# Kernel tuning notes

Measured on AMD Instinct MI355X. Metric: run time of the kernel, lower is better.

## Reference

```python
import jax, jax.numpy as jnp
import numpy as np
from jax.scipy.special import gammaln

F = 128      # n_atom_basis = n_filters
K = 25       # n_basis_functions
L = 3        # n_interactions
CUTOFF = 5.0
MAX_Z = 100
B, A, NBH = 16, 256, 64


def ssp(x):
    # shifted softplus: log(0.5*e^x + 0.5)
    return jax.nn.softplus(x) - jnp.log(2.0).astype(x.dtype)


def cosine_cutoff(r):
    return jnp.where(r < CUTOFF, 0.5 * (jnp.cos(jnp.pi * r / CUTOFF) + 1.0), 0.0)


def bernstein_basis(r):
    # ExponentialBernsteinPolynomials: Bernstein polys of exp(-r), K functions
    x = jnp.exp(-r)[..., None]                      # [..., 1]
    k = jnp.arange(K, dtype=r.dtype)
    n = jnp.asarray(K - 1, dtype=r.dtype)
    logbinom = gammaln(n + 1) - gammaln(k + 1) - gammaln(n - k + 1)
    eps = 1e-10
    return jnp.exp(logbinom + k * jnp.log(x + eps) + (n - k) * jnp.log(1.0 - x + eps))


def gather_nbh(y, neighbors):
    # y: [B, A, D], neighbors: [B, A, N] -> [B, A, N, D]
    b, a, n = neighbors.shape
    idx = neighbors.reshape(b, a * n)
    out = jnp.take_along_axis(y, idx[:, :, None], axis=1)
    return out.reshape(b, a, n, y.shape[-1])


def setup_inputs() -> dict:
    key = jax.random.key(0)
    ks = jax.random.split(key, 16)
    s = 0.05
    inp = {
        "positions": jax.random.normal(ks[0], (B, A, 3), dtype=jnp.float32) * 3.0,
        "neighbor_mask": jnp.ones((B, A, NBH), dtype=jnp.float32),
        "atom_mask": jnp.ones((B, A), dtype=jnp.float32),
        "emb": jax.random.normal(ks[1], (MAX_Z, F), dtype=jnp.float32) * s,
        "Wfs": jax.random.normal(ks[2], (L, K, F), dtype=jnp.float32) * s,
        "Wfp": jax.random.normal(ks[3], (L, K, F), dtype=jnp.float32) * s,
        "Win": jax.random.normal(ks[4], (L, F, F), dtype=jnp.float32) * s,
        "Wf2o": jax.random.normal(ks[5], (L, F, F), dtype=jnp.float32) * s,
        "bf2o": jnp.zeros((L, F), dtype=jnp.float32),
        "Wd": jax.random.normal(ks[6], (L, F, F), dtype=jnp.float32) * s,
        "bd": jnp.zeros((L, F), dtype=jnp.float32),
        "Wq": jax.random.normal(ks[7], (L, F, F), dtype=jnp.float32) * s,
        "Wk": jax.random.normal(ks[8], (L, F, F), dtype=jnp.float32) * s,
        "Wv": jax.random.normal(ks[9], (L, F, F), dtype=jnp.float32) * s,
        "atomic_numbers": jax.random.randint(ks[10], (B, A), 0, MAX_Z, dtype=jnp.int32),
        "neighbors": jax.random.randint(ks[11], (B, A, NBH), 0, A, dtype=jnp.int32),
    }
    return inp


def reference(positions, neighbor_mask, atom_mask, emb, Wfs, Wfp, Win, Wf2o, bf2o,
              Wd, bd, Wq, Wk, Wv, atomic_numbers, neighbors):
    # embedding (padding_idx=0 means Z=0 rows are just the table row; fine for ref)
    x = emb[atomic_numbers]                              # [B,A,F]

    # AtomDistances (no PBC): gather neighbor positions, distances + directions
    pos_j = gather_nbh(positions, neighbors)             # [B,A,N,3]
    rvec = pos_j - positions[:, :, None, :]
    r = jnp.sqrt(jnp.sum(rvec * rvec, axis=-1) + 1e-12) * neighbor_mask  # [B,A,N]
    dhat = rvec / (r[..., None] + 1e-9)                  # unit directions (l=1 harmonics)

    f = bernstein_basis(r)                               # [B,A,N,K]
    fc = cosine_cutoff(r) * neighbor_mask                # [B,A,N]

    for l in range(L):
        # --- LocalInteraction: angular CFConv (s + p blocks) ---
        Ws = (f @ Wfs[l]) * fc[..., None]                # [B,A,N,F]
        Wp = (f @ Wfp[l]) * fc[..., None]                # [B,A,N,F]
        y = x @ Win[l]                                   # in2f, no bias
        yj = gather_nbh(y, neighbors)                    # [B,A,N,F]
        cs = jnp.sum(yj * Ws, axis=2)                    # s-block scatter-sum [B,A,F]
        tp = jnp.einsum('banm,banf->bamf', dhat, yj * Wp)  # [B,A,3,F]
        cp = jnp.sum(tp * tp, axis=2)                    # rot-invariant p-block [B,A,F]
        v = ssp((cs + cp) @ Wf2o[l] + bf2o[l])           # f2out with shifted softplus
        v = v @ Wd[l] + bd[l]                            # interaction dense

        # --- NonLocalInteraction: masked attention ---
        xm = x * atom_mask[..., None]
        q = ssp(xm @ Wq[l])
        k = ssp(xm @ Wk[l])
        vv = ssp(xm @ Wv[l])
        logits = jnp.einsum('baf,bcf->bac', q, k) / jnp.sqrt(jnp.float32(F))
        logits = logits + (1.0 - atom_mask)[:, None, :] * (-1e9)
        att = jax.nn.softmax(logits, axis=-1)
        n = jnp.einsum('bac,bcf->baf', att, vv) * atom_mask[..., None]

        x = x + v + n                                    # residual update
    return x
```

## Files before the change

kernel.cpp:

```cpp
#include <hip/hip_runtime.h>
#include <hip/hip_bf16.h>
#include <math.h>

#define NB   16
#define NA   256
#define NNBH 64
#define NF   128
#define NK   25
#define NATOM (NB*NA)

typedef __attribute__((ext_vector_type(4))) float f32x4;
typedef __attribute__((ext_vector_type(8))) short bf16x8;

__device__ __constant__ float BINOM_C[25] = {
  1.f, 24.f, 276.f, 2024.f, 10626.f, 42504.f, 134596.f, 346104.f,
  735471.f, 1307504.f, 1961256.f, 2496144.f, 2704156.f, 2496144.f,
  1961256.f, 1307504.f, 735471.f, 346104.f, 134596.f, 42504.f,
  10626.f, 2024.f, 276.f, 24.f, 1.f
};

__device__ __forceinline__ float sspf(float x) {
  float t = (x > 20.f) ? x : log1pf(expf(x));
  return t - 0.69314718055994531f;
}
__device__ __forceinline__ unsigned short f2bf(float x) {
  __hip_bfloat16 h = __float2bfloat16(x);
  return *(unsigned short*)&h;
}

__global__ __launch_bounds__(256) void k_init(
    const float* __restrict__ Win, const float* __restrict__ Wf2o,
    const float* __restrict__ Wd, const float* __restrict__ Wq,
    const float* __restrict__ Wk, const float* __restrict__ Wv,
    const float* __restrict__ Wfs, const float* __restrict__ Wfp,
    __hip_bfloat16* __restrict__ WT, __hip_bfloat16* __restrict__ Wfb) {
  int bid = blockIdx.x, tid = threadIdx.x;
  if (bid < 1152) {
    int idx = bid * 256 + tid;
    int e = idx & 16383; int m = idx >> 14;
    int l = m / 6, wsel = m - l * 6;
    const float* src = (wsel == 0) ? Win : (wsel == 1) ? Wf2o : (wsel == 2) ? Wd
                      : (wsel == 3) ? Wq : (wsel == 4) ? Wk : Wv;
    int k = e >> 7, col = e & 127;
    WT[m * 16384 + col * 128 + k] = __float2bfloat16(src[l * NF * NF + k * NF + col]);
  } else {
    int idx = (bid - 1152) * 256 + tid;
    int k = idx & 31, f = (idx >> 5) & 127, s = (idx >> 12) & 1, l = idx >> 13;
    float v = 0.f;
    if (k < NK) v = (s ? Wfp : Wfs)[l * NK * NF + k * NF + f];
    Wfb[idx] = __float2bfloat16(v);
  }
}

template<int HV>
__global__ __launch_bounds__(256) void k_proj(
    const float* __restrict__ xg, const int* __restrict__ Z,
    const float* __restrict__ emb,
    const float* __restrict__ Cb, const float* __restrict__ Nb,
    const __hip_bfloat16* __restrict__ WTf2o_p, const float* __restrict__ bf2o_p,
    const __hip_bfloat16* __restrict__ WTd_p, const float* __restrict__ bd_p,
    const float* __restrict__ amask, const __hip_bfloat16* __restrict__ WTl,
    float* __restrict__ xout,
    __hip_bfloat16* __restrict__ ybf, __hip_bfloat16* __restrict__ Qw,
    __hip_bfloat16* __restrict__ Kw, __hip_bfloat16* __restrict__ VwT) {
  __shared__ __hip_bfloat16 hLDS[16 * 132];
  __shared__ float xLDS[16 * 133];
  int tid = threadIdx.x;
  int z = tid >> 6, l = tid & 63, lr = l & 15, lg = l >> 4;
  int rbase = blockIdx.x * 16;

  if (HV) {
    bf16x8 cfr[4];
    const float* cr = Cb + (rbase + lr) * NF;
    #pragma unroll
    for (int ks = 0; ks < 4; ks++) {
      int k0 = ks * 32 + lg * 8;
      float4 a = *(const float4*)&cr[k0];
      float4 c = *(const float4*)&cr[k0 + 4];
      bf16x8 t;
      t[0] = (short)f2bf(a.x); t[1] = (short)f2bf(a.y);
      t[2] = (short)f2bf(a.z); t[3] = (short)f2bf(a.w);
      t[4] = (short)f2bf(c.x); t[5] = (short)f2bf(c.y);
      t[6] = (short)f2bf(c.z); t[7] = (short)f2bf(c.w);
      cfr[ks] = t;
    }
    f32x4 hacc[2];
    hacc[0] = (f32x4){0.f, 0.f, 0.f, 0.f};
    hacc[1] = (f32x4){0.f, 0.f, 0.f, 0.f};
    #pragma unroll
    for (int ks = 0; ks < 4; ks++)
      #pragma unroll
      for (int j = 0; j < 2; j++) {
        bf16x8 bfr = *(const bf16x8*)(WTf2o_p + ((2 * z + j) * 16 + lr) * NF + ks * 32 + lg * 8);
        hacc[j] = __builtin_amdgcn_mfma_f32_16x16x32_bf16(cfr[ks], bfr, hacc[j], 0, 0, 0);
      }
    #pragma unroll
    for (int j = 0; j < 2; j++) {
      int col = (2 * z + j) * 16 + lr;
      float bv = bf2o_p[col];
      #pragma unroll
      for (int r = 0; r < 4; r++)
        hLDS[(4 * lg + r) * 132 + col] = __float2bfloat16(sspf(hacc[j][r] + bv));
    }
    __syncthreads();
    bf16x8 hfr[4];
    #pragma unroll
    for (int ks = 0; ks < 4; ks++)
      hfr[ks] = *(const bf16x8*)&hLDS[lr * 132 + ks * 32 + lg * 8];
    f32x4 vacc[2];
    vacc[0] = (f32x4){0.f, 0.f, 0.f, 0.f};
    vacc[1] = (f32x4){0.f, 0.f, 0.f, 0.f};
    #pragma unroll
    for (int ks = 0; ks < 4; ks++)
      #pragma unroll
      for (int j = 0; j < 2; j++) {
        bf16x8 bfr = *(const bf16x8*)(WTd_p + ((2 * z + j) * 16 + lr) * NF + ks * 32 + lg * 8);
        vacc[j] = __builtin_amdgcn_mfma_f32_16x16x32_bf16(hfr[ks], bfr, vacc[j], 0, 0, 0);
      }
    #pragma unroll
    for (int j = 0; j < 2; j++) {
      int col = (2 * z + j) * 16 + lr;
      float bv = bd_p[col];
      #pragma unroll
      for (int r = 0; r < 4; r++) {
        int row = rbase + 4 * lg + r;
        float xv = xg[row * NF + col] + vacc[j][r] + bv + Nb[row * NF + col];
        xout[row * NF + col] = xv;
        xLDS[(4 * lg + r) * 133 + col] = xv;
      }
    }
    __syncthreads();
  } else {
    int rr = tid >> 4, c0 = (tid & 15) * 8;
    int row = rbase + rr;
    const float* er = emb + Z[row] * NF;
    float4 a = *(const float4*)&er[c0];
    float4 b = *(const float4*)&er[c0 + 4];
    *(float4*)&xout[row * NF + c0] = a;
    *(float4*)&xout[row * NF + c0 + 4] = b;
    xLDS[rr * 133 + c0 + 0] = a.x; xLDS[rr * 133 + c0 + 1] = a.y;
    xLDS[rr * 133 + c0 + 2] = a.z; xLDS[rr * 133 + c0 + 3] = a.w;
    xLDS[rr * 133 + c0 + 4] = b.x; xLDS[rr * 133 + c0 + 5] = b.y;
    xLDS[rr * 133 + c0 + 6] = b.z; xLDS[rr * 133 + c0 + 7] = b.w;
    __syncthreads();
  }

  float am = (z > 0) ? amask[rbase + lr] : 1.0f;
  bf16x8 afr[4];
  #pragma unroll
  for (int ks = 0; ks < 4; ks++) {
    int k0 = ks * 32 + lg * 8;
    bf16x8 t;
    #pragma unroll
    for (int jj = 0; jj < 8; jj++)
      t[jj] = (short)f2bf(xLDS[lr * 133 + k0 + jj] * am);
    afr[ks] = t;
  }
  const __hip_bfloat16* WT = WTl + ((z == 0) ? 0 : (z + 2)) * (NF * NF);

  f32x4 acc[8];
  #pragma unroll
  for (int nt = 0; nt < 8; nt++) acc[nt] = (f32x4){0.f, 0.f, 0.f, 0.f};
  #pragma unroll
  for (int ks = 0; ks < 4; ks++)
    #pragma unroll
    for (int nt = 0; nt < 8; nt++) {
      bf16x8 bfr = *(const bf16x8*)(WT + (nt * 16 + lr) * NF + ks * 32 + lg * 8);
      acc[nt] = __builtin_amdgcn_mfma_f32_16x16x32_bf16(afr[ks], bfr, acc[nt], 0, 0, 0);
    }

  if (z < 3) {
    __hip_bfloat16* out = (z == 0) ? ybf : (z == 1) ? Qw : Kw;
    #pragma unroll
    for (int nt = 0; nt < 8; nt++) {
      int col = nt * 16 + lr;
      #pragma unroll
      for (int r = 0; r < 4; r++) {
        int orow = rbase + lg * 4 + r;
        float o = acc[nt][r];
        if (z > 0) o = sspf(o);
        out[orow * NF + col] = __float2bfloat16(o);
      }
    }
  } else {
    int b = blockIdx.x >> 4;
    int ar0 = (blockIdx.x & 15) * 16 + lg * 4;
    #pragma unroll
    for (int nt = 0; nt < 8; nt++) {
      int col = nt * 16 + lr;
      #pragma unroll
      for (int r = 0; r < 4; r++)
        VwT[(b * NF + col) * NA + ar0 + r] = __float2bfloat16(sspf(acc[nt][r]));
    }
  }
}

__global__ __launch_bounds__(256) void k_fa(
    const __hip_bfloat16* __restrict__ ybf, const int* __restrict__ nbrs,
    const float* __restrict__ pos, const float* __restrict__ nmask,
    const __hip_bfloat16* __restrict__ Wfb_l, float* __restrict__ cOut,
    const __hip_bfloat16* __restrict__ Qw, const __hip_bfloat16* __restrict__ Kw,
    const __hip_bfloat16* __restrict__ VwT, const float* __restrict__ amask,
    float* __restrict__ Nb) {
  __shared__ char smem[23296];
  int tid = threadIdx.x;
  int lane = tid & 63, w = tid >> 6, lr = lane & 15, lg = lane >> 4;

  if (blockIdx.x < 4096) {
    __hip_bfloat16* FF  = (__hip_bfloat16*)smem;
    __hip_bfloat16* yjl = (__hip_bfloat16*)(smem + 5120);
    float (*d3l)[4]     = (float(*)[4])(smem + 22016);
    int* jl             = (int*)(smem + 23040);
    int atom = blockIdx.x, brow = atom & ~(NA - 1);

    {
      int n = tid & 63;
      int j = nbrs[atom * NNBH + n];
      float px = pos[(brow + j) * 3 + 0] - pos[atom * 3 + 0];
      float py = pos[(brow + j) * 3 + 1] - pos[atom * 3 + 1];
      float pz = pos[(brow + j) * 3 + 2] - pos[atom * 3 + 2];
      float m = nmask[atom * NNBH + n];
      float r = sqrtf(px * px + py * py + pz * pz + 1e-12f) * m;
      float inv = 1.0f / (r + 1e-9f);
      float fc = (r < 5.0f) ? (0.5f * cosf(0.62831853071795865f * r) + 0.5f) * m : 0.0f;
      float xe = expf(-r);
      float l1 = log2f(xe + 1e-10f);
      float l2 = log2f(1.0f - xe + 1e-10f);
      if (tid < NNBH) {
        jl[n] = j;
        d3l[n][0] = 0.f;
        d3l[n][1] = px * inv;
        d3l[n][2] = py * inv;
        d3l[n][3] = pz * inv;
      }
      int kq = tid >> 6;
      bf16x8 v;
      #pragma unroll
      for (int j8 = 0; j8 < 8; j8++) {
        int k = kq * 8 + j8;
        float val = 0.f;
        if (k < NK)
          val = BINOM_C[k] * exp2f((float)k * l1 + (float)(24 - k) * l2) * fc;
        v[j8] = (short)f2bf(val);
      }
      *(bf16x8*)&FF[n * 40 + kq * 8] = v;
    }
    __syncthreads();

    {
      int n = tid >> 2, c0 = (tid & 3) * 32;
      const __hip_bfloat16* src = &ybf[(brow + jl[n]) * NF + c0];
      #pragma unroll
      for (int i = 0; i < 4; i++) {
        uint4 u = *(const uint4*)(src + i * 8);
        uint2* dst = (uint2*)&yjl[n * 132 + c0 + i * 8];
        dst[0] = make_uint2(u.x, u.y);
        dst[1] = make_uint2(u.z, u.w);
      }
    }
    __syncthreads();

    bf16x8 af[4];
    #pragma unroll
    for (int mt = 0; mt < 4; mt++)
      af[mt] = *(bf16x8*)&FF[(16 * mt + lr) * 40 + lg * 8];

    f32x4 as_[4][2], ap_[4][2];
    #pragma unroll
    for (int mt = 0; mt < 4; mt++)
      #pragma unroll
      for (int nt2 = 0; nt2 < 2; nt2++) {
        as_[mt][nt2] = (f32x4){0.f, 0.f, 0.f, 0.f};
        ap_[mt][nt2] = (f32x4){0.f, 0.f, 0.f, 0.f};
      }
    #pragma unroll
    for (int nt2 = 0; nt2 < 2; nt2++) {
      int col = 32 * w + 16 * nt2 + lr;
      bf16x8 bs = *(const bf16x8*)&Wfb_l[col * 32 + lg * 8];
      bf16x8 bp = *(const bf16x8*)&Wfb_l[(128 + col) * 32 + lg * 8];
      #pragma unroll
      for (int mt = 0; mt < 4; mt++) {
        as_[mt][nt2] = __builtin_amdgcn_mfma_f32_16x16x32_bf16(af[mt], bs, as_[mt][nt2], 0, 0, 0);
        ap_[mt][nt2] = __builtin_amdgcn_mfma_f32_16x16x32_bf16(af[mt], bp, ap_[mt][nt2], 0, 0, 0);
      }
    }

    float qs[2] = {0.f, 0.f}, q1[2] = {0.f, 0.f}, q2[2] = {0.f, 0.f}, q3[2] = {0.f, 0.f};
    #pragma unroll
    for (int mt = 0; mt < 4; mt++) {
      #pragma unroll
      for (int r = 0; r < 4; r++) {
        int n = 16 * mt + 4 * lg + r;
        float4 dv = *(const float4*)&d3l[n][0];
        #pragma unroll
        for (int nt2 = 0; nt2 < 2; nt2++) {
          int f = 32 * w + 16 * nt2 + lr;
          float yv = __bfloat162float(yjl[n * 132 + f]);
          qs[nt2] += yv * as_[mt][nt2][r];
          float pw = yv * ap_[mt][nt2][r];
          q1[nt2] += dv.y * pw;
          q2[nt2] += dv.z * pw;
          q3[nt2] += dv.w * pw;
        }
      }
    }
    #pragma unroll
    for (int nt2 = 0; nt2 < 2; nt2++) {
      float a = qs[nt2], b1 = q1[nt2], b2 = q2[nt2], b3 = q3[nt2];
      a  += __shfl_xor(a, 16);  a  += __shfl_xor(a, 32);
      b1 += __shfl_xor(b1, 16); b1 += __shfl_xor(b1, 32);
      b2 += __shfl_xor(b2, 16); b2 += __shfl_xor(b2, 32);
      b3 += __shfl_xor(b3, 16); b3 += __shfl_xor(b3, 32);
      if (lg == 0)
        cOut[atom * NF + 32 * w + 16 * nt2 + lr] = a + b1 * b1 + b2 * b2 + b3 * b3;
    }
  } else {
    __hip_bfloat16* Plds = (__hip_bfloat16*)smem;
    float* mwl = (float*)(smem + 8320);
    float* swl = (float*)(smem + 8576);
    int bb = blockIdx.x - 4096;
    int b = bb >> 4, qt = bb & 15;
    int qbase = b * NA + qt * 16;
    const float scale = 0.08838834764831845f;

    bf16x8 qf[4];
    #pragma unroll
    for (int ks = 0; ks < 4; ks++)
      qf[ks] = *(const bf16x8*)&Qw[(qbase + lr) * NF + ks * 32 + lg * 8];

    f32x4 sacc[4];
    #pragma unroll
    for (int ntc = 0; ntc < 4; ntc++) sacc[ntc] = (f32x4){0.f, 0.f, 0.f, 0.f};
    #pragma unroll
    for (int ks = 0; ks < 4; ks++)
      #pragma unroll
      for (int ntc = 0; ntc < 4; ntc++) {
        bf16x8 kf = *(const bf16x8*)&Kw[(b * NA + w * 64 + ntc * 16 + lr) * NF + ks * 32 + lg * 8];
        sacc[ntc] = __builtin_amdgcn_mfma_f32_16x16x32_bf16(qf[ks], kf, sacc[ntc], 0, 0, 0);
      }

    float kam[4];
    #pragma unroll
    for (int ntc = 0; ntc < 4; ntc++)
      kam[ntc] = (1.0f - amask[b * NA + w * 64 + ntc * 16 + lr]) * (-1e9f);

    #pragma unroll
    for (int r = 0; r < 4; r++) {
      float lv[4], cm = -1e30f;
      #pragma unroll
      for (int ntc = 0; ntc < 4; ntc++) {
        lv[ntc] = sacc[ntc][r] * scale + kam[ntc];
        cm = fmaxf(cm, lv[ntc]);
      }
      cm = fmaxf(cm, __shfl_xor(cm, 1)); cm = fmaxf(cm, __shfl_xor(cm, 2));
      cm = fmaxf(cm, __shfl_xor(cm, 4)); cm = fmaxf(cm, __shfl_xor(cm, 8));
      float ps = 0.f;
      #pragma unroll
      for (int ntc = 0; ntc < 4; ntc++) {
        float p = expf(lv[ntc] - cm);
        Plds[(4 * lg + r) * 260 + w * 64 + ntc * 16 + lr] = __float2bfloat16(p);
        ps += p;
      }
      ps += __shfl_xor(ps, 1); ps += __shfl_xor(ps, 2);
      ps += __shfl_xor(ps, 4); ps += __shfl_xor(ps, 8);
      if (lr == 0) {
        mwl[w * 16 + 4 * lg + r] = cm;
        swl[w * 16 + 4 * lg + r] = ps;
      }
    }
    __syncthreads();

    float ec[4][4], inv_[4];
    #pragma unroll
    for (int r = 0; r < 4; r++) {
      int row = 4 * lg + r;
      float m0 = mwl[row], m1 = mwl[16 + row], m2 = mwl[32 + row], m3 = mwl[48 + row];
      float M = fmaxf(fmaxf(m0, m1), fmaxf(m2, m3));
      float e0 = expf(m0 - M), e1 = expf(m1 - M), e2 = expf(m2 - M), e3 = expf(m3 - M);
      ec[0][r] = e0; ec[1][r] = e1; ec[2][r] = e2; ec[3][r] = e3;
      float s = swl[row] * e0 + swl[16 + row] * e1 + swl[32 + row] * e2 + swl[48 + row] * e3;
      inv_[r] = amask[qbase + row] / s;
    }

    f32x4 O[2];
    O[0] = (f32x4){0.f, 0.f, 0.f, 0.f};
    O[1] = (f32x4){0.f, 0.f, 0.f, 0.f};
    #pragma unroll
    for (int c = 0; c < 4; c++) {
      bf16x8 pf[2];
      #pragma unroll
      for (int s2 = 0; s2 < 2; s2++)
        pf[s2] = *(const bf16x8*)&Plds[lr * 260 + c * 64 + s2 * 32 + lg * 8];
      f32x4 tc[2];
      tc[0] = (f32x4){0.f, 0.f, 0.f, 0.f};
      tc[1] = (f32x4){0.f, 0.f, 0.f, 0.f};
      #pragma unroll
      for (int s2 = 0; s2 < 2; s2++)
        #pragma unroll
        for (int j = 0; j < 2; j++) {
          bf16x8 vf = *(const bf16x8*)&VwT[(b * NF + (2 * w + j) * 16 + lr) * NA + c * 64 + s2 * 32 + lg * 8];
          tc[j] = __builtin_amdgcn_mfma_f32_16x16x32_bf16(pf[s2], vf, tc[j], 0, 0, 0);
        }
      #pragma unroll
      for (int j = 0; j < 2; j++)
        #pragma unroll
        for (int r = 0; r < 4; r++)
          O[j][r] += ec[c][r] * tc[j][r];
    }

    #pragma unroll
    for (int r = 0; r < 4; r++) {
      int q = qbase + 4 * lg + r;
      #pragma unroll
      for (int j = 0; j < 2; j++) {
        int col = (2 * w + j) * 16 + lr;
        Nb[q * NF + col] = O[j][r] * inv_[r];
      }
    }
  }
}

__global__ __launch_bounds__(256) void k_final(
    const float* __restrict__ Cb, const float* __restrict__ Nb,
    const __hip_bfloat16* __restrict__ WTf2o_p, const float* __restrict__ bf2o_p,
    const __hip_bfloat16* __restrict__ WTd_p, const float* __restrict__ bd_p,
    float* __restrict__ x) {
  __shared__ __hip_bfloat16 hLDS[16 * 132];
  int tid = threadIdx.x;
  int z = tid >> 6, l = tid & 63, lr = l & 15, lg = l >> 4;
  int rbase = blockIdx.x * 16;

  bf16x8 cfr[4];
  const float* cr = Cb + (rbase + lr) * NF;
  #pragma unroll
  for (int ks = 0; ks < 4; ks++) {
    int k0 = ks * 32 + lg * 8;
    float4 a = *(const float4*)&cr[k0];
    float4 c = *(const float4*)&cr[k0 + 4];
    bf16x8 t;
    t[0] = (short)f2bf(a.x); t[1] = (short)f2bf(a.y);
    t[2] = (short)f2bf(a.z); t[3] = (short)f2bf(a.w);
    t[4] = (short)f2bf(c.x); t[5] = (short)f2bf(c.y);
    t[6] = (short)f2bf(c.z); t[7] = (short)f2bf(c.w);
    cfr[ks] = t;
  }
  f32x4 hacc[2];
  hacc[0] = (f32x4){0.f, 0.f, 0.f, 0.f};
  hacc[1] = (f32x4){0.f, 0.f, 0.f, 0.f};
  #pragma unroll
  for (int ks = 0; ks < 4; ks++)
    #pragma unroll
    for (int j = 0; j < 2; j++) {
      bf16x8 bfr = *(const bf16x8*)(WTf2o_p + ((2 * z + j) * 16 + lr) * NF + ks * 32 + lg * 8);
      hacc[j] = __builtin_amdgcn_mfma_f32_16x16x32_bf16(cfr[ks], bfr, hacc[j], 0, 0, 0);
    }
  #pragma unroll
  for (int j = 0; j < 2; j++) {
    int col = (2 * z + j) * 16 + lr;
    float bv = bf2o_p[col];
    #pragma unroll
    for (int r = 0; r < 4; r++)
      hLDS[(4 * lg + r) * 132 + col] = __float2bfloat16(sspf(hacc[j][r] + bv));
  }
  __syncthreads();
  bf16x8 hfr[4];
  #pragma unroll
  for (int ks = 0; ks < 4; ks++)
    hfr[ks] = *(const bf16x8*)&hLDS[lr * 132 + ks * 32 + lg * 8];
  f32x4 vacc[2];
  vacc[0] = (f32x4){0.f, 0.f, 0.f, 0.f};
  vacc[1] = (f32x4){0.f, 0.f, 0.f, 0.f};
  #pragma unroll
  for (int ks = 0; ks < 4; ks++)
    #pragma unroll
    for (int j = 0; j < 2; j++) {
      bf16x8 bfr = *(const bf16x8*)(WTd_p + ((2 * z + j) * 16 + lr) * NF + ks * 32 + lg * 8);
      vacc[j] = __builtin_amdgcn_mfma_f32_16x16x32_bf16(hfr[ks], bfr, vacc[j], 0, 0, 0);
    }
  #pragma unroll
  for (int j = 0; j < 2; j++) {
    int col = (2 * z + j) * 16 + lr;
    float bv = bd_p[col];
    #pragma unroll
    for (int r = 0; r < 4; r++) {
      int row = rbase + 4 * lg + r;
      x[row * NF + col] += vacc[j][r] + bv + Nb[row * NF + col];
    }
  }
}

extern "C" void kernel_launch(void* const* d_in, const int* in_sizes, int n_in,
                              void* d_out, int out_size, void* d_ws, size_t ws_size,
                              hipStream_t stream) {
  const float* pos   = (const float*)d_in[0];
  const float* nmask = (const float*)d_in[1];
  const float* amask = (const float*)d_in[2];
  const float* emb   = (const float*)d_in[3];
  const float* Wfs   = (const float*)d_in[4];
  const float* Wfp   = (const float*)d_in[5];
  const float* Win   = (const float*)d_in[6];
  const float* Wf2o  = (const float*)d_in[7];
  const float* bf2o  = (const float*)d_in[8];
  const float* Wd    = (const float*)d_in[9];
  const float* bd    = (const float*)d_in[10];
  const float* Wq    = (const float*)d_in[11];
  const float* Wk    = (const float*)d_in[12];
  const float* Wv    = (const float*)d_in[13];
  const int*   Z     = (const int*)d_in[14];
  const int*   nbrs  = (const int*)d_in[15];

  float* x = (float*)d_out;
  float* wsf = (float*)d_ws;
  const int S = NATOM * NF;
  float* Cb = wsf;
  float* Nb = wsf + S;
  __hip_bfloat16* ybf = (__hip_bfloat16*)(wsf + 2 * S);
  __hip_bfloat16* Qw  = ybf + S;
  __hip_bfloat16* Kw  = Qw + S;
  __hip_bfloat16* VwT = Kw + S;
  __hip_bfloat16* WT  = VwT + S;
  __hip_bfloat16* Wfb = WT + 18 * 16384;

  k_init<<<dim3(1248), dim3(256), 0, stream>>>(
      Win, Wf2o, Wd, Wq, Wk, Wv, Wfs, Wfp, WT, Wfb);

  for (int l = 0; l < 3; l++) {
    const __hip_bfloat16* WTl = WT + l * 6 * 16384;
    if (l == 0)
      k_proj<0><<<dim3(256), dim3(256), 0, stream>>>(
          nullptr, Z, emb, nullptr, nullptr, nullptr, nullptr, nullptr, nullptr,
          amask, WTl, x, ybf, Qw, Kw, VwT);
    else {
      const __hip_bfloat16* WTp = WT + (l - 1) * 6 * 16384;
      k_proj<1><<<dim3(256), dim3(256), 0, stream>>>(
          x, nullptr, nullptr, Cb, Nb, WTp + 16384, bf2o + (l - 1) * NF,
          WTp + 2 * 16384, bd + (l - 1) * NF, amask, WTl, x, ybf, Qw, Kw, VwT);
    }
    k_fa<<<dim3(4096 + 256), dim3(256), 0, stream>>>(
        ybf, nbrs, pos, nmask, Wfb + l * 8192, Cb, Qw, Kw, VwT, amask, Nb);
  }
  const __hip_bfloat16* WT2 = WT + 2 * 6 * 16384;
  k_final<<<dim3(256), dim3(256), 0, stream>>>(
      Cb, Nb, WT2 + 16384, bf2o + 2 * NF, WT2 + 2 * 16384, bd + 2 * NF, x);
}
```

Before: 191.5 us.

## Fuse all stages into one persistent cooperative kernel with grid syncs

Replaces the eight separate kernel launches (init, per-layer projection and filter/attention, final) with a single persistent cooperative kernel. Work items are distributed over a grid capped at 1024 blocks, with grid-wide barriers between stages. This targets launch overhead and inter-kernel gaps, at the cost of grid.sync latency, lost occupancy from the grid cap and launch bounds, and host-side occupancy queries on every call. A fallback path keeps separate launches if the cooperative launch fails.

New measurement: 612.4 us. +219.8%, slower.

```diff
diff --git a/kernel.cpp b/kernel.cpp
--- a/kernel.cpp
+++ b/kernel.cpp
@@ -1,6 +1,9 @@
 #include <hip/hip_runtime.h>
+#include <hip/hip_cooperative_groups.h>
 #include <hip/hip_bf16.h>
 #include <math.h>
+
+namespace cg = cooperative_groups;
 
 #define NB   16
 #define NA   256
@@ -8,6 +11,7 @@
 #define NF   128
 #define NK   25
 #define NATOM (NB*NA)
+#define SMEM_BYTES 23296
 
 typedef __attribute__((ext_vector_type(4))) float f32x4;
 typedef __attribute__((ext_vector_type(8))) short bf16x8;
@@ -28,50 +32,48 @@
   return *(unsigned short*)&h;
 }
 
-__global__ __launch_bounds__(256) void k_init(
-    const float* __restrict__ Win, const float* __restrict__ Wf2o,
-    const float* __restrict__ Wd, const float* __restrict__ Wq,
-    const float* __restrict__ Wk, const float* __restrict__ Wv,
-    const float* __restrict__ Wfs, const float* __restrict__ Wfp,
-    __hip_bfloat16* __restrict__ WT, __hip_bfloat16* __restrict__ Wfb) {
-  int bid = blockIdx.x, tid = threadIdx.x;
-  if (bid < 1152) {
-    int idx = bid * 256 + tid;
+struct Params {
+  const float *pos, *nmask, *amask, *emb;
+  const float *Wfs, *Wfp, *Win, *Wf2o, *bf2o, *Wd, *bd, *Wq, *Wk, *Wv;
+  const int *Z, *nbrs;
+  float *x;
+  float *Cb, *Nb;
+  __hip_bfloat16 *ybf, *Qw, *Kw, *VwT, *WT, *Wfb;
+};
+
+__device__ __forceinline__ void dev_init(int i, int tid, const Params& p) {
+  if (i < 1152) {
+    int idx = i * 256 + tid;
     int e = idx & 16383; int m = idx >> 14;
     int l = m / 6, wsel = m - l * 6;
-    const float* src = (wsel == 0) ? Win : (wsel == 1) ? Wf2o : (wsel == 2) ? Wd
-                      : (wsel == 3) ? Wq : (wsel == 4) ? Wk : Wv;
+    const float* src = (wsel == 0) ? p.Win : (wsel == 1) ? p.Wf2o : (wsel == 2) ? p.Wd
+                      : (wsel == 3) ? p.Wq : (wsel == 4) ? p.Wk : p.Wv;
     int k = e >> 7, col = e & 127;
-    WT[m * 16384 + col * 128 + k] = __float2bfloat16(src[l * NF * NF + k * NF + col]);
+    p.WT[m * 16384 + col * 128 + k] = __float2bfloat16(src[l * NF * NF + k * NF + col]);
   } else {
-    int idx = (bid - 1152) * 256 + tid;
+    int idx = (i - 1152) * 256 + tid;
     int k = idx & 31, f = (idx >> 5) & 127, s = (idx >> 12) & 1, l = idx >> 13;
     float v = 0.f;
-    if (k < NK) v = (s ? Wfp : Wfs)[l * NK * NF + k * NF + f];
-    Wfb[idx] = __float2bfloat16(v);
-  }
-}
-
-template<int HV>
-__global__ __launch_bounds__(256) void k_proj(
-    const float* __restrict__ xg, const int* __restrict__ Z,
-    const float* __restrict__ emb,
-    const float* __restrict__ Cb, const float* __restrict__ Nb,
-    const __hip_bfloat16* __restrict__ WTf2o_p, const float* __restrict__ bf2o_p,
-    const __hip_bfloat16* __restrict__ WTd_p, const float* __restrict__ bd_p,
-    const float* __restrict__ amask, const __hip_bfloat16* __restrict__ WTl,
-    float* __restrict__ xout,
-    __hip_bfloat16* __restrict__ ybf, __hip_bfloat16* __restrict__ Qw,
-    __hip_bfloat16* __restrict__ Kw, __hip_bfloat16* __restrict__ VwT) {
-  __shared__ __hip_bfloat16 hLDS[16 * 132];
-  __shared__ float xLDS[16 * 133];
-  int tid = threadIdx.x;
-  int z = tid >> 6, l = tid & 63, lr = l & 15, lg = l >> 4;
-  int rbase = blockIdx.x * 16;
-
-  if (HV) {
+    if (k < NK) v = (s ? p.Wfp : p.Wfs)[l * NK * NF + k * NF + f];
+    p.Wfb[idx] = __float2bfloat16(v);
+  }
+}
+
+__device__ void dev_proj(int l, int tile, int tid, char* smem, const Params& p) {
+  __hip_bfloat16* hLDS = (__hip_bfloat16*)smem;
+  float* xLDS = (float*)(smem + 4224);
+  int z = tid >> 6, ln = tid & 63, lr = ln & 15, lg = ln >> 4;
+  int rbase = tile * 16;
+
+  if (l > 0) {
+    const __hip_bfloat16* WTp = p.WT + (l - 1) * 6 * 16384;
+    const __hip_bfloat16* WTf2o_p = WTp + 16384;
+    const __hip_bfloat16* WTd_p = WTp + 2 * 16384;
+    const float* bf2o_p = p.bf2o + (l - 1) * NF;
+    const float* bd_p = p.bd + (l - 1) * NF;
+
     bf16x8 cfr[4];
-    const float* cr = Cb + (rbase + lr) * NF;
+    const float* cr = p.Cb + (rbase + lr) * NF;
     #pragma unroll
     for (int ks = 0; ks < 4; ks++) {
       int k0 = ks * 32 + lg * 8;
@@ -124,8 +126,8 @@
       #pragma unroll
       for (int r = 0; r < 4; r++) {
         int row = rbase + 4 * lg + r;
-        float xv = xg[row * NF + col] + vacc[j][r] + bv + Nb[row * NF + col];
-        xout[row * NF + col] = xv;
+        float xv = p.x[row * NF + col] + vacc[j][r] + bv + p.Nb[row * NF + col];
+        p.x[row * NF + col] = xv;
         xLDS[(4 * lg + r) * 133 + col] = xv;
       }
     }
@@ -133,11 +135,11 @@
   } else {
     int rr = tid >> 4, c0 = (tid & 15) * 8;
     int row = rbase + rr;
-    const float* er = emb + Z[row] * NF;
+    const float* er = p.emb + p.Z[row] * NF;
     float4 a = *(const float4*)&er[c0];
     float4 b = *(const float4*)&er[c0 + 4];
-    *(float4*)&xout[row * NF + c0] = a;
-    *(float4*)&xout[row * NF + c0 + 4] = b;
+    *(float4*)&p.x[row * NF + c0] = a;
+    *(float4*)&p.x[row * NF + c0 + 4] = b;
     xLDS[rr * 133 + c0 + 0] = a.x; xLDS[rr * 133 + c0 + 1] = a.y;
     xLDS[rr * 133 + c0 + 2] = a.z; xLDS[rr * 133 + c0 + 3] = a.w;
     xLDS[rr * 133 + c0 + 4] = b.x; xLDS[rr * 133 + c0 + 5] = b.y;
@@ -145,7 +147,8 @@
     __syncthreads();
   }
 
-  float am = (z > 0) ? amask[rbase + lr] : 1.0f;
+  const __hip_bfloat16* WTl = p.WT + l * 6 * 16384;
+  float am = (z > 0) ? p.amask[rbase + lr] : 1.0f;
   bf16x8 afr[4];
   #pragma unroll
   for (int ks = 0; ks < 4; ks++) {
@@ -170,7 +173,7 @@
     }
 
   if (z < 3) {
-    __hip_bfloat16* out = (z == 0) ? ybf : (z == 1) ? Qw : Kw;
+    __hip_bfloat16* out = (z == 0) ? p.ybf : (z == 1) ? p.Qw : p.Kw;
     #pragma unroll
     for (int nt = 0; nt < 8; nt++) {
       int col = nt * 16 + lr;
@@ -183,255 +186,247 @@
       }
     }
   } else {
-    int b = blockIdx.x >> 4;
-    int ar0 = (blockIdx.x & 15) * 16 + lg * 4;
+    int b = tile >> 4;
+    int ar0 = (tile & 15) * 16 + lg * 4;
     #pragma unroll
     for (int nt = 0; nt < 8; nt++) {
       int col = nt * 16 + lr;
       #pragma unroll
       for (int r = 0; r < 4; r++)
-        VwT[(b * NF + col) * NA + ar0 + r] = __float2bfloat16(sspf(acc[nt][r]));
-    }
-  }
-}
-
-__global__ __launch_bounds__(256) void k_fa(
-    const __hip_bfloat16* __restrict__ ybf, const int* __restrict__ nbrs,
-    const float* __restrict__ pos, const float* __restrict__ nmask,
-    const __hip_bfloat16* __restrict__ Wfb_l, float* __restrict__ cOut,
-    const __hip_bfloat16* __restrict__ Qw, const __hip_bfloat16* __restrict__ Kw,
-    const __hip_bfloat16* __restrict__ VwT, const float* __restrict__ amask,
-    float* __restrict__ Nb) {
-  __shared__ char smem[23296];
-  int tid = threadIdx.x;
+        p.VwT[(b * NF + col) * NA + ar0 + r] = __float2bfloat16(sspf(acc[nt][r]));
+    }
+  }
+}
+
+__device__ void dev_filter(int atom, int tid, char* smem, const Params& p,
+                           const __hip_bfloat16* __restrict__ Wfb_l) {
+  __hip_bfloat16* FF  = (__hip_bfloat16*)smem;
+  __hip_bfloat16* yjl = (__hip_bfloat16*)(smem + 5120);
+  float (*d3l)[4]     = (float(*)[4])(smem + 22016);
+  int* jl             = (int*)(smem + 23040);
+  int brow = atom & ~(NA - 1);
   int lane = tid & 63, w = tid >> 6, lr = lane & 15, lg = lane >> 4;
 
-  if (blockIdx.x < 4096) {
-    __hip_bfloat16* FF  = (__hip_bfloat16*)smem;
-    __hip_bfloat16* yjl = (__hip_bfloat16*)(smem + 5120);
-    float (*d3l)[4]     = (float(*)[4])(smem + 22016);
-    int* jl             = (int*)(smem + 23040);
-    int atom = blockIdx.x, brow = atom & ~(NA - 1);
-
-    {
-      int n = tid & 63;
-      int j = nbrs[atom * NNBH + n];
-      float px = pos[(brow + j) * 3 + 0] - pos[atom * 3 + 0];
-      float py = pos[(brow + j) * 3 + 1] - pos[atom * 3 + 1];
-      float pz = pos[(brow + j) * 3 + 2] - pos[atom * 3 + 2];
-      float m = nmask[atom * NNBH + n];
-      float r = sqrtf(px * px + py * py + pz * pz + 1e-12f) * m;
-      float inv = 1.0f / (r + 1e-9f);
-      float fc = (r < 5.0f) ? (0.5f * cosf(0.62831853071795865f * r) + 0.5f) * m : 0.0f;
-      float xe = expf(-r);
-      float l1 = log2f(xe + 1e-10f);
-      float l2 = log2f(1.0f - xe + 1e-10f);
-      if (tid < NNBH) {
-        jl[n] = j;
-        d3l[n][0] = 0.f;
-        d3l[n][1] = px * inv;
-        d3l[n][2] = py * inv;
-        d3l[n][3] = pz * inv;
+  {
+    int n = tid & 63;
+    int j = p.nbrs[atom * NNBH + n];
+    float px = p.pos[(brow + j) * 3 + 0] - p.pos[atom * 3 + 0];
+    float py = p.pos[(brow + j) * 3 + 1] - p.pos[atom * 3 + 1];
+    float pz = p.pos[(brow + j) * 3 + 2] - p.pos[atom * 3 + 2];
+    float m = p.nmask[atom * NNBH + n];
+    float r = sqrtf(px * px + py * py + pz * pz + 1e-12f) * m;
+    float inv = 1.0f / (r + 1e-9f);
+    float fc = (r < 5.0f) ? (0.5f * cosf(0.62831853071795865f * r) + 0.5f) * m : 0.0f;
+    float xe = expf(-r);
+    float l1 = log2f(xe + 1e-10f);
+    float l2 = log2f(1.0f - xe + 1e-10f);
+    if (tid < NNBH) {
+      jl[n] = j;
+      d3l[n][0] = 0.f;
+      d3l[n][1] = px * inv;
+      d3l[n][2] = py * inv;
+      d3l[n][3] = pz * inv;
+    }
+    int kq = tid >> 6;
+    bf16x8 v;
+    #pragma unroll
+    for (int j8 = 0; j8 < 8; j8++) {
+      int k = kq * 8 + j8;
+      float val = 0.f;
+      if (k < NK)
+        val = BINOM_C[k] * exp2f((float)k * l1 + (float)(24 - k) * l2) * fc;
+      v[j8] = (short)f2bf(val);
+    }
+    *(bf16x8*)&FF[n * 40 + kq * 8] = v;
+  }
+  __syncthreads();
+
+  {
+    int n = tid >> 2, c0 = (tid & 3) * 32;
+    const __hip_bfloat16* src = &p.ybf[(brow + jl[n]) * NF + c0];
+    #pragma unroll
+    for (int i = 0; i < 4; i++) {
+      uint4 u = *(const uint4*)(src + i * 8);
+      uint2* dst = (uint2*)&yjl[n * 132 + c0 + i * 8];
+      dst[0] = make_uint2(u.x, u.y);
+      dst[1] = make_uint2(u.z, u.w);
+    }
+  }
+  __syncthreads();
+
+  bf16x8 af[4];
+  #pragma unroll
+  for (int mt = 0; mt < 4; mt++)
+    af[mt] = *(bf16x8*)&FF[(16 * mt + lr) * 40 + lg * 8];
+
+  f32x4 as_[4][2], ap_[4][2];
+  #pragma unroll
+  for (int mt = 0; mt < 4; mt++)
+    #pragma unroll
+    for (int nt2 = 0; nt2 < 2; nt2++) {
+      as_[mt][nt2] = (f32x4){0.f, 0.f, 0.f, 0.f};
+      ap_[mt][nt2] = (f32x4){0.f, 0.f, 0.f, 0.f};
+    }
+  #pragma unroll
+  for (int nt2 = 0; nt2 < 2; nt2++) {
+    int col = 32 * w + 16 * nt2 + lr;
+    bf16x8 bs = *(const bf16x8*)&Wfb_l[col * 32 + lg * 8];
+    bf16x8 bp = *(const bf16x8*)&Wfb_l[(128 + col) * 32 + lg * 8];
+    #pragma unroll
+    for (int mt = 0; mt < 4; mt++) {
+      as_[mt][nt2] = __builtin_amdgcn_mfma_f32_16x16x32_bf16(af[mt], bs, as_[mt][nt2], 0, 0, 0);
+      ap_[mt][nt2] = __builtin_amdgcn_mfma_f32_16x16x32_bf16(af[mt], bp, ap_[mt][nt2], 0, 0, 0);
+    }
+  }
+
+  float qs[2] = {0.f, 0.f}, q1[2] = {0.f, 0.f}, q2[2] = {0.f, 0.f}, q3[2] = {0.f, 0.f};
+  #pragma unroll
+  for (int mt = 0; mt < 4; mt++) {
+    #pragma unroll
+    for (int r = 0; r < 4; r++) {
+      int n = 16 * mt + 4 * lg + r;
+      float4 dv = *(const float4*)&d3l[n][0];
+      #pragma unroll
+      for (int nt2 = 0; nt2 < 2; nt2++) {
+        int f = 32 * w + 16 * nt2 + lr;
+        float yv = __bfloat162float(yjl[n * 132 + f]);
+        qs[nt2] += yv * as_[mt][nt2][r];
+        float pw = yv * ap_[mt][nt2][r];
+        q1[nt2] += dv.y * pw;
+        q2[nt2] += dv.z * pw;
+        q3[nt2] += dv.w * pw;
       }
-      int kq = tid >> 6;
-      bf16x8 v;
-      #pragma unroll
-      for (int j8 = 0; j8 < 8; j8++) {
-        int k = kq * 8 + j8;
-        float val = 0.f;
-        if (k < NK)
-          val = BINOM_C[k] * exp2f((float)k * l1 + (float)(24 - k) * l2) * fc;
-        v[j8] = (short)f2bf(val);
+    }
+  }
+  #pragma unroll
+  for (int nt2 = 0; nt2 < 2; nt2++) {
+    float a = qs[nt2], b1 = q1[nt2], b2 = q2[nt2], b3 = q3[nt2];
+    a  += __shfl_xor(a, 16);  a  += __shfl_xor(a, 32);
+    b1 += __shfl_xor(b1, 16); b1 += __shfl_xor(b1, 32);
+    b2 += __shfl_xor(b2, 16); b2 += __shfl_xor(b2, 32);
+    b3 += __shfl_xor(b3, 16); b3 += __shfl_xor(b3, 32);
+    if (lg == 0)
+      p.Cb[atom * NF + 32 * w + 16 * nt2 + lr] = a + b1 * b1 + b2 * b2 + b3 * b3;
+  }
+}
+
+__device__ void dev_attn(int bb, int tid, char* smem, const Params& p) {
+  __hip_bfloat16* Plds = (__hip_bfloat16*)smem;
+  float* mwl = (float*)(smem + 8320);
+  float* swl = (float*)(smem + 8576);
+  int lane = tid & 63, w = tid >> 6, lr = lane & 15, lg = lane >> 4;
+  int b = bb >> 4, qt = bb & 15;
+  int qbase = b * NA + qt * 16;
+  const float scale = 0.08838834764831845f;
+
+  bf16x8 qf[4];
+  #pragma unroll
+  for (int ks = 0; ks < 4; ks++)
+    qf[ks] = *(const bf16x8*)&p.Qw[(qbase + lr) * NF + ks * 32 + lg * 8];
+
+  f32x4 sacc[4];
+  #pragma unroll
+  for (int ntc = 0; ntc < 4; ntc++) sacc[ntc] = (f32x4){0.f, 0.f, 0.f, 0.f};
+  #pragma unroll
+  for (int ks = 0; ks < 4; ks++)
+    #pragma unroll
+    for (int ntc = 0; ntc < 4; ntc++) {
+      bf16x8 kf = *(const bf16x8*)&p.Kw[(b * NA + w * 64 + ntc * 16 + lr) * NF + ks * 32 + lg * 8];
+      sacc[ntc] = __builtin_amdgcn_mfma_f32_16x16x32_bf16(qf[ks], kf, sacc[ntc], 0, 0, 0);
+    }
+
+  float kam[4];
+  #pragma unroll
+  for (int ntc = 0; ntc < 4; ntc++)
+    kam[ntc] = (1.0f - p.amask[b * NA + w * 64 + ntc * 16 + lr]) * (-1e9f);
+
+  #pragma unroll
+  for (int r = 0; r < 4; r++) {
+    float lv[4], cm = -1e30f;
+    #pragma unroll
+    for (int ntc = 0; ntc < 4; ntc++) {
+      lv[ntc] = sacc[ntc][r] * scale + kam[ntc];
+      cm = fmaxf(cm, lv[ntc]);
+    }
+    cm = fmaxf(cm, __shfl_xor(cm, 1)); cm = fmaxf(cm, __shfl_xor(cm, 2));
+    cm = fmaxf(cm, __shfl_xor(cm, 4)); cm = fmaxf(cm, __shfl_xor(cm, 8));
+    float ps = 0.f;
+    #pragma unroll
+    for (int ntc = 0; ntc < 4; ntc++) {
+      float pp = expf(lv[ntc] - cm);
+      Plds[(4 * lg + r) * 260 + w * 64 + ntc * 16 + lr] = __float2bfloat16(pp);
+      ps += pp;
+    }
+    ps += __shfl_xor(ps, 1); ps += __shfl_xor(ps, 2);
+    ps += __shfl_xor(ps, 4); ps += __shfl_xor(ps, 8);
+    if (lr == 0) {
+      mwl[w * 16 + 4 * lg + r] = cm;
+      swl[w * 16 + 4 * lg + r] = ps;
+    }
+  }
+  __syncthreads();
+
+  float ec[4][4], inv_[4];
+  #pragma unroll
+  for (int r = 0; r < 4; r++) {
+    int row = 4 * lg + r;
+    float m0 = mwl[row], m1 = mwl[16 + row], m2 = mwl[32 + row], m3 = mwl[48 + row];
+    float M = fmaxf(fmaxf(m0, m1), fmaxf(m2, m3));
+    float e0 = expf(m0 - M), e1 = expf(m1 - M), e2 = expf(m2 - M), e3 = expf(m3 - M);
+    ec[0][r] = e0; ec[1][r] = e1; ec[2][r] = e2; ec[3][r] = e3;
+    float s = swl[row] * e0 + swl[16 + row] * e1 + swl[32 + row] * e2 + swl[48 + row] * e3;
+    inv_[r] = p.amask[qbase + row] / s;
+  }
+
+  f32x4 O[2];
+  O[0] = (f32x4){0.f, 0.f, 0.f, 0.f};
+  O[1] = (f32x4){0.f, 0.f, 0.f, 0.f};
+  #pragma unroll
+  for (int c = 0; c < 4; c++) {
+    bf16x8 pf[2];
+    #pragma unroll
+    for (int s2 = 0; s2 < 2; s2++)
+      pf[s2] = *(const bf16x8*)&Plds[lr * 260 + c * 64 + s2 * 32 + lg * 8];
+    f32x4 tc[2];
+    tc[0] = (f32x4){0.f, 0.f, 0.f, 0.f};
+    tc[1] = (f32x4){0.f, 0.f, 0.f, 0.f};
+    #pragma unroll
+    for (int s2 = 0; s2 < 2; s2++)
+      #pragma unroll
+      for (int j = 0; j < 2; j++) {
+        bf16x8 vf = *(const bf16x8*)&p.VwT[(b * NF + (2 * w + j) * 16 + lr) * NA + c * 64 + s2 * 32 + lg * 8];
+        tc[j] = __builtin_amdgcn_mfma_f32_16x16x32_bf16(pf[s2], vf, tc[j], 0, 0, 0);
       }
-      *(bf16x8*)&FF[n * 40 + kq * 8] = v;
-    }
-    __syncthreads();
-
-    {
-      int n = tid >> 2, c0 = (tid & 3) * 32;
-      const __hip_bfloat16* src = &ybf[(brow + jl[n]) * NF + c0];
-      #pragma unroll
-      for (int i = 0; i < 4; i++) {
-        uint4 u = *(const uint4*)(src + i * 8);
-        uint2* dst = (uint2*)&yjl[n * 132 + c0 + i * 8];
-        dst[0] = make_uint2(u.x, u.y);
-        dst[1] = make_uint2(u.z, u.w);
-      }
-    }
-    __syncthreads();
-
-    bf16x8 af[4];
-    #pragma unroll
-    for (int mt = 0; mt < 4; mt++)
-      af[mt] = *(bf16x8*)&FF[(16 * mt + lr) * 40 + lg * 8];
-
-    f32x4 as_[4][2], ap_[4][2];
-    #pragma unroll
-    for (int mt = 0; mt < 4; mt++)
-      #pragma unroll
-      for (int nt2 = 0; nt2 < 2; nt2++) {
-        as_[mt][nt2] = (f32x4){0.f, 0.f, 0.f, 0.f};
-        ap_[mt][nt2] = (f32x4){0.f, 0.f, 0.f, 0.f};
-      }
-    #pragma unroll
-    for (int nt2 = 0; nt2 < 2; nt2++) {
-      int col = 32 * w + 16 * nt2 + lr;
-      bf16x8 bs = *(const bf16x8*)&Wfb_l[col * 32 + lg * 8];
-      bf16x8 bp = *(const bf16x8*)&Wfb_l[(128 + col) * 32 + lg * 8];
-      #pragma unroll
-      for (int mt = 0; mt < 4; mt++) {
-        as_[mt][nt2] = __builtin_amdgcn_mfma_f32_16x16x32_bf16(af[mt], bs, as_[mt][nt2], 0, 0, 0);
-        ap_[mt][nt2] = __builtin_amdgcn_mfma_f32_16x16x32_bf16(af[mt], bp, ap_[mt][nt2], 0, 0, 0);
-      }
-    }
-
-    float qs[2] = {0.f, 0.f}, q1[2] = {0.f, 0.f}, q2[2] = {0.f, 0.f}, q3[2] = {0.f, 0.f};
-    #pragma unroll
-    for (int mt = 0; mt < 4; mt++) {
-      #pragma unroll
-      for (int r = 0; r < 4; r++) {
-        int n = 16 * mt + 4 * lg + r;
-        float4 dv = *(const float4*)&d3l[n][0];
-        #pragma unroll
-        for (int nt2 = 0; nt2 < 2; nt2++) {
-          int f = 32 * w + 16 * nt2 + lr;
-          float yv = __bfloat162float(yjl[n * 132 + f]);
-          qs[nt2] += yv * as_[mt][nt2][r];
-          float pw = yv * ap_[mt][nt2][r];
-          q1[nt2] += dv.y * pw;
-          q2[nt2] += dv.z * pw;
-          q3[nt2] += dv.w * pw;
-        }
-      }
-    }
-    #pragma unroll
-    for (int nt2 = 0; nt2 < 2; nt2++) {
-      float a = qs[nt2], b1 = q1[nt2], b2 = q2[nt2], b3 = q3[nt2];
-      a  += __shfl_xor(a, 16);  a  += __shfl_xor(a, 32);
-      b1 += __shfl_xor(b1, 16); b1 += __shfl_xor(b1, 32);
-      b2 += __shfl_xor(b2, 16); b2 += __shfl_xor(b2, 32);
-      b3 += __shfl_xor(b3, 16); b3 += __shfl_xor(b3, 32);
-      if (lg == 0)
-        cOut[atom * NF + 32 * w + 16 * nt2 + lr] = a + b1 * b1 + b2 * b2 + b3 * b3;
-    }
-  } else {
-    __hip_bfloat16* Plds = (__hip_bfloat16*)smem;
-    float* mwl = (float*)(smem + 8320);
-    float* swl = (float*)(smem + 8576);
-    int bb = blockIdx.x - 4096;
-    int b = bb >> 4, qt = bb & 15;
-    int qbase = b * NA + qt * 16;
-    const float scale = 0.08838834764831845f;
-
-    bf16x8 qf[4];
-    #pragma unroll
-    for (int ks = 0; ks < 4; ks++)
-      qf[ks] = *(const bf16x8*)&Qw[(qbase + lr) * NF + ks * 32 + lg * 8];
-
-    f32x4 sacc[4];
-    #pragma unroll
-    for (int ntc = 0; ntc < 4; ntc++) sacc[ntc] = (f32x4){0.f, 0.f, 0.f, 0.f};
-    #pragma unroll
-    for (int ks = 0; ks < 4; ks++)
-      #pragma unroll
-      for (int ntc = 0; ntc < 4; ntc++) {
-        bf16x8 kf = *(const bf16x8*)&Kw[(b * NA + w * 64 + ntc * 16 + lr) * NF + ks * 32 + lg * 8];
-        sacc[ntc] = __builtin_amdgcn_mfma_f32_16x16x32_bf16(qf[ks], kf, sacc[ntc], 0, 0, 0);
-      }
-
-    float kam[4];
-    #pragma unroll
-    for (int ntc = 0; ntc < 4; ntc++)
-      kam[ntc] = (1.0f - amask[b * NA + w * 64 + ntc * 16 + lr]) * (-1e9f);
-
-    #pragma unroll
-    for (int r = 0; r < 4; r++) {
-      float lv[4], cm = -1e30f;
-      #pragma unroll
-      for (int ntc = 0; ntc < 4; ntc++) {
-        lv[ntc] = sacc[ntc][r] * scale + kam[ntc];
-        cm = fmaxf(cm, lv[ntc]);
-      }
-      cm = fmaxf(cm, __shfl_xor(cm, 1)); cm = fmaxf(cm, __shfl_xor(cm, 2));
-      cm = fmaxf(cm, __shfl_xor(cm, 4)); cm = fmaxf(cm, __shfl_xor(cm, 8));
-      float ps = 0.f;
-      #pragma unroll
-      for (int ntc = 0; ntc < 4; ntc++) {
-        float p = expf(lv[ntc] - cm);
-        Plds[(4 * lg + r) * 260 + w * 64 + ntc * 16 + lr] = __float2bfloat16(p);
-        ps += p;
-      }
-      ps += __shfl_xor(ps, 1); ps += __shfl_xor(ps, 2);
-      ps += __shfl_xor(ps, 4); ps += __shfl_xor(ps, 8);
-      if (lr == 0) {
-        mwl[w * 16 + 4 * lg + r] = cm;
-        swl[w * 16 + 4 * lg + r] = ps;
-      }
-    }
-    __syncthreads();
-
-    float ec[4][4], inv_[4];
-    #pragma unroll
-    for (int r = 0; r < 4; r++) {
-      int row = 4 * lg + r;
-      float m0 = mwl[row], m1 = mwl[16 + row], m2 = mwl[32 + row], m3 = mwl[48 + row];
-      float M = fmaxf(fmaxf(m0, m1), fmaxf(m2, m3));
-      float e0 = expf(m0 - M), e1 = expf(m1 - M), e2 = expf(m2 - M), e3 = expf(m3 - M);
-      ec[0][r] = e0; ec[1][r] = e1; ec[2][r] = e2; ec[3][r] = e3;
-      float s = swl[row] * e0 + swl[16 + row] * e1 + swl[32 + row] * e2 + swl[48 + row] * e3;
-      inv_[r] = amask[qbase + row] / s;
-    }
-
-    f32x4 O[2];
-    O[0] = (f32x4){0.f, 0.f, 0.f, 0.f};
-    O[1] = (f32x4){0.f, 0.f, 0.f, 0.f};
-    #pragma unroll
-    for (int c = 0; c < 4; c++) {
-      bf16x8 pf[2];
-      #pragma unroll
-      for (int s2 = 0; s2 < 2; s2++)
-        pf[s2] = *(const bf16x8*)&Plds[lr * 260 + c * 64 + s2 * 32 + lg * 8];
-      f32x4 tc[2];
-      tc[0] = (f32x4){0.f, 0.f, 0.f, 0.f};
-      tc[1] = (f32x4){0.f, 0.f, 0.f, 0.f};
-      #pragma unroll
-      for (int s2 = 0; s2 < 2; s2++)
-        #pragma unroll
-        for (int j = 0; j < 2; j++) {
-          bf16x8 vf = *(const bf16x8*)&VwT[(b * NF + (2 * w + j) * 16 + lr) * NA + c * 64 + s2 * 32 + lg * 8];
-          tc[j] = __builtin_amdgcn_mfma_f32_16x16x32_bf16(pf[s2], vf, tc[j], 0, 0, 0);
-        }
-      #pragma unroll
-      for (int j = 0; j < 2; j++)
-        #pragma unroll
-        for (int r = 0; r < 4; r++)
-          O[j][r] += ec[c][r] * tc[j][r];
-    }
-
-    #pragma unroll
-    for (int r = 0; r < 4; r++) {
-      int q = qbase + 4 * lg + r;
-      #pragma unroll
-      for (int j = 0; j < 2; j++) {
-        int col = (2 * w + j) * 16 + lr;
-        Nb[q * NF + col] = O[j][r] * inv_[r];
-      }
-    }
-  }
-}
-
-__global__ __launch_bounds__(256) void k_final(
-    const float* __restrict__ Cb, const float* __restrict__ Nb,
-    const __hip_bfloat16* __restrict__ WTf2o_p, const float* __restrict__ bf2o_p,
-    const __hip_bfloat16* __restrict__ WTd_p, const float* __restrict__ bd_p,
-    float* __restrict__ x) {
-  __shared__ __hip_bfloat16 hLDS[16 * 132];
-  int tid = threadIdx.x;
-  int z = tid >> 6, l = tid & 63, lr = l & 15, lg = l >> 4;
-  int rbase = blockIdx.x * 16;
+    #pragma unroll
+    for (int j = 0; j < 2; j++)
+      #pragma unroll
+      for (int r = 0; r < 4; r++)
+        O[j][r] += ec[c][r] * tc[j][r];
+  }
+
+  #pragma unroll
+  for (int r = 0; r < 4; r++) {
+    int q = qbase + 4 * lg + r;
+    #pragma unroll
+    for (int j = 0; j < 2; j++) {
+      int col = (2 * w + j) * 16 + lr;
+      p.Nb[q * NF + col] = O[j][r] * inv_[r];
+    }
+  }
+}
+
+__device__ void dev_final(int tile, int tid, char* smem, const Params& p) {
+  __hip_bfloat16* hLDS = (__hip_bfloat16*)smem;
+  const __hip_bfloat16* WT2 = p.WT + 2 * 6 * 16384;
+  const __hip_bfloat16* WTf2o_p = WT2 + 16384;
+  const __hip_bfloat16* WTd_p = WT2 + 2 * 16384;
+  const float* bf2o_p = p.bf2o + 2 * NF;
+  const float* bd_p = p.bd + 2 * NF;
+  int z = tid >> 6, ln = tid & 63, lr = ln & 15, lg = ln >> 4;
+  int rbase = tile * 16;
 
   bf16x8 cfr[4];
-  const float* cr = Cb + (rbase + lr) * NF;
+  const float* cr = p.Cb + (rbase + lr) * NF;
   #pragma unroll
   for (int ks = 0; ks < 4; ks++) {
     int k0 = ks * 32 + lg * 8;
@@ -484,62 +479,121 @@
     #pragma unroll
     for (int r = 0; r < 4; r++) {
       int row = rbase + 4 * lg + r;
-      x[row * NF + col] += vacc[j][r] + bv + Nb[row * NF + col];
-    }
-  }
+      p.x[row * NF + col] += vacc[j][r] + bv + p.Nb[row * NF + col];
+    }
+  }
+}
+
+__global__ __launch_bounds__(256, 3) void k_mega(Params p) {
+  cg::grid_group grid = cg::this_grid();
+  __shared__ char smem[SMEM_BYTES];
+  int bid = blockIdx.x, tid = threadIdx.x;
+  int G = gridDim.x;
+
+  for (int i = bid; i < 1248; i += G)
+    dev_init(i, tid, p);
+  grid.sync();
+
+  for (int l = 0; l < 3; l++) {
+    for (int t = bid; t < 256; t += G) {
+      __syncthreads();
+      dev_proj(l, t, tid, smem, p);
+    }
+    grid.sync();
+
+    const __hip_bfloat16* Wfb_l = p.Wfb + l * 8192;
+    for (int wi = bid; wi < 4352; wi += G) {
+      __syncthreads();
+      if (wi < 4096) dev_filter(wi, tid, smem, p, Wfb_l);
+      else           dev_attn(wi - 4096, tid, smem, p);
+    }
+    grid.sync();
+  }
+
+  for (int t = bid; t < 256; t += G) {
+    __syncthreads();
+    dev_final(t, tid, smem, p);
+  }
+}
+
+__global__ __launch_bounds__(256) void k_init_g(Params p) {
+  dev_init(blockIdx.x, threadIdx.x, p);
+}
+__global__ __launch_bounds__(256) void k_proj_g(Params p, int l) {
+  __shared__ char smem[SMEM_BYTES];
+  dev_proj(l, blockIdx.x, threadIdx.x, smem, p);
+}
+__global__ __launch_bounds__(256) void k_fa_g(Params p, int l) {
+  __shared__ char smem[SMEM_BYTES];
+  if (blockIdx.x < 4096)
+    dev_filter(blockIdx.x, threadIdx.x, smem, p, p.Wfb + l * 8192);
+  else
+    dev_attn(blockIdx.x - 4096, threadIdx.x, smem, p);
+}
+__global__ __launch_bounds__(256) void k_final_g(Params p) {
+  __shared__ char smem[SMEM_BYTES];
+  dev_final(blockIdx.x, threadIdx.x, smem, p);
 }
 
 extern "C" void kernel_launch(void* const* d_in, const int* in_sizes, int n_in,
                               void* d_out, int out_size, void* d_ws, size_t ws_size,
                               hipStream_t stream) {
-  const float* pos   = (const float*)d_in[0];
-  const float* nmask = (const float*)d_in[1];
-  const float* amask = (const float*)d_in[2];
-  const float* emb   = (const float*)d_in[3];
-  const float* Wfs   = (const float*)d_in[4];
-  const float* Wfp   = (const float*)d_in[5];
-  const float* Win   = (const float*)d_in[6];
-  const float* Wf2o  = (const float*)d_in[7];
-  const float* bf2o  = (const float*)d_in[8];
-  const float* Wd    = (const float*)d_in[9];
-  const float* bd    = (const float*)d_in[10];
-  const float* Wq    = (const float*)d_in[11];
-  const float* Wk    = (const float*)d_in[12];
-  const float* Wv    = (const float*)d_in[13];
-  const int*   Z     = (const int*)d_in[14];
-  const int*   nbrs  = (const int*)d_in[15];
-
-  float* x = (float*)d_out;
+  Params prm;
+  prm.pos   = (const float*)d_in[0];
+  prm.nmask = (const float*)d_in[1];
+  prm.amask = (const float*)d_in[2];
+  prm.emb   = (const float*)d_in[3];
+  prm.Wfs   = (const float*)d_in[4];
+  prm.Wfp   = (const float*)d_in[5];
+  prm.Win   = (const float*)d_in[6];
+  prm.Wf2o  = (const float*)d_in[7];
+  prm.bf2o  = (const float*)d_in[8];
+  prm.Wd    = (const float*)d_in[9];
+  prm.bd    = (const float*)d_in[10];
+  prm.Wq    = (const float*)d_in[11];
+  prm.Wk    = (const float*)d_in[12];
+  prm.Wv    = (const float*)d_in[13];
+  prm.Z     = (const int*)d_in[14];
+  prm.nbrs  = (const int*)d_in[15];
+
   float* wsf = (float*)d_ws;
   const int S = NATOM * NF;
-  float* Cb = wsf;
-  float* Nb = wsf + S;
-  __hip_bfloat16* ybf = (__hip_bfloat16*)(wsf + 2 * S);
-  __hip_bfloat16* Qw  = ybf + S;
-  __hip_bfloat16* Kw  = Qw + S;
-  __hip_bfloat16* VwT = Kw + S;
-  __hip_bfloat16* WT  = VwT + S;
-  __hip_bfloat16* Wfb = WT + 18 * 16384;
-
-  k_init<<<dim3(1248), dim3(256), 0, stream>>>(
-      Win, Wf2o, Wd, Wq, Wk, Wv, Wfs, Wfp, WT, Wfb);
-
-  for (int l = 0; l < 3; l++) {
-    const __hip_bfloat16* WTl = WT + l * 6 * 16384;
-    if (l == 0)
-      k_proj<0><<<dim3(256), dim3(256), 0, stream>>>(
-          nullptr, Z, emb, nullptr, nullptr, nullptr, nullptr, nullptr, nullptr,
-          amask, WTl, x, ybf, Qw, Kw, VwT);
-    else {
-      const __hip_bfloat16* WTp = WT + (l - 1) * 6 * 16384;
-      k_proj<1><<<dim3(256), dim3(256), 0, stream>>>(
-          x, nullptr, nullptr, Cb, Nb, WTp + 16384, bf2o + (l - 1) * NF,
-          WTp + 2 * 16384, bd + (l - 1) * NF, amask, WTl, x, ybf, Qw, Kw, VwT);
-    }
-    k_fa<<<dim3(4096 + 256), dim3(256), 0, stream>>>(
-        ybf, nbrs, pos, nmask, Wfb + l * 8192, Cb, Qw, Kw, VwT, amask, Nb);
-  }
-  const __hip_bfloat16* WT2 = WT + 2 * 6 * 16384;
-  k_final<<<dim3(256), dim3(256), 0, stream>>>(
-      Cb, Nb, WT2 + 16384, bf2o + 2 * NF, WT2 + 2 * 16384, bd + 2 * NF, x);
-}
+  prm.x   = (float*)d_out;
+  prm.Cb  = wsf;
+  prm.Nb  = wsf + S;
+  prm.ybf = (__hip_bfloat16*)(wsf + 2 * S);
+  prm.Qw  = prm.ybf + S;
+  prm.Kw  = prm.Qw + S;
+  prm.VwT = prm.Kw + S;
+  prm.WT  = prm.VwT + S;
+  prm.Wfb = prm.WT + 18 * 16384;
+
+  int dev = 0;
+  hipGetDevice(&dev);
+  int numCU = 256;
+  hipDeviceGetAttribute(&numCU, hipDeviceAttributeMultiprocessorCount, dev);
+  int maxActive = 0;
+  hipError_t qerr = hipOccupancyMaxActiveBlocksPerMultiprocessor(
+      &maxActive, (const void*)k_mega, 256, 0);
+
+  bool launched = false;
+  if (qerr == hipSuccess && maxActive > 0) {
+    int grid = maxActive * numCU;
+    if (grid > 1024) grid = 1024;
+    if (grid >= 64) {
+      void* args[] = { &prm };
+      hipError_t lerr = hipLaunchCooperativeKernel(
+          (const void*)k_mega, dim3(grid), dim3(256), args, 0, stream);
+      launched = (lerr == hipSuccess);
+    }
+  }
+
+  if (!launched) {
+    k_init_g<<<dim3(1248), dim3(256), 0, stream>>>(prm);
+    for (int l = 0; l < 3; l++) {
+      k_proj_g<<<dim3(256), dim3(256), 0, stream>>>(prm, l);
+      k_fa_g<<<dim3(4352), dim3(256), 0, stream>>>(prm, l);
+    }
+    k_final_g<<<dim3(256), dim3(256), 0, stream>>>(prm);
+  }
+}
```
